# Performance work log

Hardware: AMD Instinct MI355X
Metric: run time of the kernel (lower is better)

Reference implementation:

```python
import jax, jax.numpy as jnp
import numpy as np
from jax import lax

IMG_SIZE = 640
STRIDES = (8, 16, 32)
NA = 3          # anchors per level
NC = 80         # classes
CONF_THRESH = 0.001
NMS_THRESH = 0.6
ANCHORS = np.array([[10,13],[16,30],[33,23],[30,61],[62,45],[59,119],[116,90],[156,198],[373,326]], np.float32).reshape(3, 3, 2)

def _make_grids():
    gs, st, aw = [], [], []
    for i, s in enumerate(STRIDES):
        hs = ws = IMG_SIZE // s
        gy, gx = np.meshgrid(np.arange(hs), np.arange(ws), indexing='ij')
        gxy = np.stack([gx, gy], -1).astype(np.float32).reshape(1, hs*ws, 1, 2)
        gs.append(gxy)
        st.append(np.full((1, hs*ws, NA, 2), s, np.float32))
        aw.append(np.tile(ANCHORS[i][None], (hs*ws, 1, 1)))
    return (np.concatenate(gs, 1), np.concatenate(st, 1), np.concatenate(aw, 0)[None])

GRID_CELL, STRIDE_T, ANCH_WH = _make_grids()  # [1,HW,1,2], [1,HW,3,2], [1,HW,3,2]

def _nms_classaware(boxes, score, valid):
    # Greedy NMS, class-aware via coordinate offset already applied to boxes.
    # Faithful to the numpy baseline: w,h = max(1e-28, .), areas without +1.
    x1, y1, x2, y2 = boxes[:, 0], boxes[:, 1], boxes[:, 2], boxes[:, 3]
    areas = (x2 - x1) * (y2 - y1)
    order = jnp.argsort(-score)
    N = boxes.shape[0]
    def body(i, state):
        supp, keep = state
        idx = order[i]
        active = jnp.logical_and(jnp.logical_not(supp[idx]), valid[idx])
        keep = keep.at[idx].set(active)
        xx1 = jnp.maximum(x1[idx], x1)
        yy1 = jnp.maximum(y1[idx], y1)
        xx2 = jnp.minimum(x2[idx], x2)
        yy2 = jnp.minimum(y2[idx], y2)
        w = jnp.maximum(1e-28, xx2 - xx1)
        h = jnp.maximum(1e-28, yy2 - yy1)
        inter = w * h
        iou = inter / (areas[idx] + areas - inter)
        newsupp = jnp.logical_and(iou > NMS_THRESH, active)
        newsupp = newsupp.at[idx].set(False)
        return jnp.logical_or(supp, newsupp), keep
    supp0 = jnp.zeros((N,), bool)
    keep0 = jnp.zeros((N,), bool)
    _, keep = lax.fori_loop(0, N, body, (supp0, keep0))
    return keep

def _decode_and_nms(pred_s, pred_m, pred_l):
    objs, clss, regs = [], [], []
    for pred in (pred_s, pred_m, pred_l):
        B, C, H, W = pred.shape
        p = pred.transpose(0, 2, 3, 1).reshape(B, H*W, C)
        objs.append(p[..., :NA].reshape(B, H*W*NA, 1))
        clss.append(p[..., NA:NA*(1+NC)].reshape(B, H*W*NA, NC))
        regs.append(p[..., NA*(1+NC):].reshape(B, H*W, NA, 4))
    obj_pred = jnp.concatenate(objs, axis=1)   # [B, N, 1]
    cls_pred = jnp.concatenate(clss, axis=1)   # [B, N, NC]
    reg_pred = jnp.concatenate(regs, axis=1)   # [B, HW, 3, 4]
    grid = jnp.asarray(GRID_CELL)
    stride = jnp.asarray(STRIDE_T)
    anch = jnp.asarray(ANCH_WH)
    B = reg_pred.shape[0]
    c_xy = (jax.nn.sigmoid(reg_pred[..., :2]) + grid) * stride
    b_wh = jnp.exp(reg_pred[..., 2:]) * anch
    xywh = jnp.concatenate([c_xy, b_wh], -1).reshape(B, -1, 4)
    x1y1 = xywh[..., :2] - xywh[..., 2:] / 2
    x2y2 = xywh[..., :2] + xywh[..., 2:] / 2
    boxes = jnp.clip(jnp.concatenate([x1y1, x2y2], -1) / IMG_SIZE, 0.0, 1.0)[0]  # [N,4]
    obj_s = jax.nn.sigmoid(obj_pred)[0]                     # [N,1]
    scores_all = jax.nn.softmax(cls_pred[0], axis=1) * obj_s  # [N,NC]
    cls_ind = jnp.argmax(scores_all, axis=1)                # [N]
    score = jnp.max(scores_all, axis=1)                     # [N]
    valid = score >= CONF_THRESH
    # class-aware NMS: offset normalized boxes by 2*class so classes never overlap
    boxes_off = boxes + cls_ind[:, None].astype(boxes.dtype) * 2.0
    keep = _nms_classaware(lax.stop_gradient(boxes_off), lax.stop_gradient(score), valid)
    out = jnp.concatenate([
        boxes,                                    # 4 cols
        score[:, None],                           # 1 col
        cls_ind[:, None].astype(boxes.dtype),     # 1 col (non-diff)
        keep[:, None].astype(boxes.dtype),        # 1 col (non-diff)
    ], axis=1)                                    # [N, 7]
    return out

def setup_inputs() -> dict:
    key = jax.random.key(0)
    k1, k2, k3 = jax.random.split(key, 3)
    return {
        'pred_s': jax.random.normal(k1, (1, 255, 80, 80), jnp.float32),
        'pred_m': jax.random.normal(k2, (1, 255, 40, 40), jnp.float32),
        'pred_l': jax.random.normal(k3, (1, 255, 20, 20), jnp.float32),
    }

def reference(pred_s, pred_m, pred_l):
    return _decode_and_nms(pred_s, pred_m, pred_l)
```

## Files before the change

kernel.cpp:

```cpp
#include <hip/hip_runtime.h>
#include <cstdint>

#define NPRED 25200
#define NPOS  8400
#define NCLS  80
#define CAP   512
#define MW    8
#define NCHUNK 132

__device__ __forceinline__ float sigmoidf_(float x) { return 1.0f / (1.0f + expf(-x)); }

__global__ __launch_bounds__(64, 2) void decode_kernel(
    const float* __restrict__ ps, const float* __restrict__ pm, const float* __restrict__ pl,
    float* __restrict__ out,
    float4* __restrict__ g_boxin, uint64_t* __restrict__ g_key)
{
    int chunk = blockIdx.x;
    int a     = blockIdx.y;
    int t     = threadIdx.x;

    const float* p; int HW, W, base, si; float stride; int w0;
    if (chunk < 100)      { p = ps; HW = 6400; W = 80; stride = 8.f;  base = 0;    si = 0; w0 = chunk * 64; }
    else if (chunk < 125) { p = pm; HW = 1600; W = 40; stride = 16.f; base = 6400; si = 1; w0 = (chunk - 100) * 64; }
    else                  { p = pl; HW = 400;  W = 20; stride = 32.f; base = 8000; si = 2; w0 = (chunk - 125) * 64; }

    int local = w0 + t;
    bool valid = local < HW;
    int lclamp = valid ? local : (HW - 1);

    const float* cbase = p + (size_t)(3 + a * NCLS) * HW + lclamp;
    float v[NCLS];
#pragma unroll
    for (int c = 0; c < NCLS; c++) v[c] = cbase[(size_t)c * HW];

    float objl = p[(size_t)a * HW + lclamp];
    const float* rb = p + (size_t)(3 + 3 * NCLS + a * 4) * HW + lclamp;
    float tx = rb[0], ty = rb[(size_t)HW], tw = rb[(size_t)2 * HW], th = rb[(size_t)3 * HW];

    float m = -INFINITY;
#pragma unroll
    for (int c = 0; c < NCLS; c++) m = fmaxf(m, v[c]);
    float s = 0.f; float beste = -1.f; int bi = 0;
#pragma unroll
    for (int c = 0; c < NCLS; c++) {
        float e = expf(v[c] - m);
        s += e;
        if (e > beste) { beste = e; bi = c; }
    }
    float obj = sigmoidf_(objl);
    float best = beste / s * obj;

    if (!valid) return;

    const float AW[9] = {10.f,16.f,33.f, 30.f,62.f,59.f, 116.f,156.f,373.f};
    const float AH[9] = {13.f,30.f,23.f, 61.f,45.f,119.f, 90.f,198.f,326.f};
    float aw = AW[si*3 + a], ah = AH[si*3 + a];

    int y = local / W;
    int x = local - y * W;
    float cx = (sigmoidf_(tx) + (float)x) * stride;
    float cy = (sigmoidf_(ty) + (float)y) * stride;
    float bw = expf(tw) * aw;
    float bh = expf(th) * ah;
    float x1 = fminf(fmaxf((cx - bw / 2.f) / 640.f, 0.f), 1.f);
    float y1 = fminf(fmaxf((cy - bh / 2.f) / 640.f, 0.f), 1.f);
    float x2 = fminf(fmaxf((cx + bw / 2.f) / 640.f, 0.f), 1.f);
    float y2 = fminf(fmaxf((cy + bh / 2.f) / 640.f, 0.f), 1.f);

    int g = (base + local) * 3 + a;
    float clsf = (float)bi;
    float* o = out + (size_t)g * 7;
    o[0] = x1; o[1] = y1; o[2] = x2; o[3] = y2;
    o[4] = best; o[5] = clsf; o[6] = 0.f;

    if (best >= 0.001f) {
        float off2 = clsf * 2.0f;
        g_boxin[g] = make_float4(x1 + off2, y1 + off2, x2 + off2, y2 + off2);
        unsigned u = __float_as_uint(best);
        u = (u & 0x80000000u) ? ~u : (u | 0x80000000u);
        g_key[g] = ((uint64_t)bi << 47) | ((uint64_t)(~u) << 15) | (uint64_t)g;
    } else {
        g_key[g] = (uint64_t)127 << 47;
    }
}

#define BUCKET2(kv)                                                       \
    {                                                                     \
        bool m0 = (int)((kv).x >> 47) == c;                               \
        bool m1 = (int)((kv).y >> 47) == c;                               \
        unsigned long long b0 = __ballot(m0);                             \
        unsigned long long b1 = __ballot(m1);                             \
        int total = __popcll(b0) + __popcll(b1);                          \
        int bs = 0;                                                       \
        if (lane == 0 && total) bs = atomicAdd(&ln_s, total);             \
        bs = __shfl(bs, 0);                                               \
        unsigned long long lower = ((unsigned long long)1 << lane) - 1;   \
        int off0 = bs + __popcll(b0 & lower);                             \
        int off1 = bs + __popcll(b0) + __popcll(b1 & lower);              \
        if (m0 && off0 < CAP) key_s[off0] = (kv).x;                       \
        if (m1 && off1 < CAP) key_s[off1] = (kv).y;                       \
    }

__global__ __launch_bounds__(1024, 4) void nms_fused_kernel(
    const uint64_t* __restrict__ g_key, const float4* __restrict__ g_boxin,
    float* __restrict__ out)
{
    int c = blockIdx.x;
    int tid = threadIdx.x;

    __shared__ alignas(16) uint64_t key_s[CAP];
    __shared__ float4   boxu_s[CAP];
    __shared__ float4   sbox_s[CAP + 64];
    __shared__ int      sg_s[CAP];
    __shared__ uint64_t mask_s[MW * CAP];
    __shared__ int      ln_s;

    if (tid == 0) ln_s = 0;
    __syncthreads();

    {
        int lane = tid & 63;
        const ulonglong2* kp = (const ulonglong2*)g_key;
        const int HALF = NPRED / 2;
        const int R2 = HALF >> 11;
        for (int r = 0; r < R2; r++) {
            int i0 = (r << 11) + tid;
            ulonglong2 ka = kp[i0];
            ulonglong2 kb = kp[i0 + 1024];
            BUCKET2(ka);
            BUCKET2(kb);
        }
        int ti = (R2 << 11) + tid;
        if (ti < HALF) {
            ulonglong2 ka = kp[ti];
            BUCKET2(ka);
        }
    }
    __syncthreads();
    int n = ln_s; if (n > CAP) n = CAP;
    if (n == 0) return;
    int nw = (n + 63) >> 6;

    for (int i = tid; i < n; i += 1024)
        boxu_s[i] = g_boxin[key_s[i] & 0x7FFF];
    for (int i = n + tid; i < n + 64; i += 1024)
        sbox_s[i] = make_float4(3e30f, 3e30f, 3e30f, 3e30f);
    __syncthreads();

    for (int i0 = 0; i0 < n; i0 += 256) {
        int item = i0 + (tid >> 2);
        int sub  = tid & 3;
        bool act = item < n;
        int r = 0;
        uint64_t k = 0;
        if (act) {
            k = key_s[item];
            int nq = (((n + 3) >> 2) + 1) & ~1;
            int lo = sub * nq; if (lo > n) lo = n;
            int hi = lo + nq;  if (hi > n) hi = n;
            int jj = lo;
            for (; jj + 8 <= hi; jj += 8) {
                ulonglong2 p0 = *(const ulonglong2*)&key_s[jj];
                ulonglong2 p1 = *(const ulonglong2*)&key_s[jj + 2];
                ulonglong2 p2 = *(const ulonglong2*)&key_s[jj + 4];
                ulonglong2 p3 = *(const ulonglong2*)&key_s[jj + 6];
                r += (p0.x < k) + (p0.y < k) + (p1.x < k) + (p1.y < k)
                   + (p2.x < k) + (p2.y < k) + (p3.x < k) + (p3.y < k);
            }
            for (; jj + 2 <= hi; jj += 2) {
                ulonglong2 p0 = *(const ulonglong2*)&key_s[jj];
                r += (p0.x < k) + (p0.y < k);
            }
            if (jj < hi) r += (key_s[jj] < k);
        }
        r += __shfl_xor(r, 1);
        r += __shfl_xor(r, 2);
        if (act && sub == 0) {
            sbox_s[r] = boxu_s[item];
            sg_s[r]   = (int)(k & 0x7FFF);
        }
    }
    __syncthreads();

    {
        int wid   = tid >> 6;
        int lane2 = tid & 63;
        int T = nw * (nw + 1) / 2;
        for (int t = wid; t < T; t += 16) {
            int w = 0, acc = 0;
            while (t >= acc + w + 1) { acc += w + 1; w++; }
            int ib = t - acc;
            int i  = (ib << 6) + lane2;
            float4 b4 = sbox_s[i];
            float Ai = (b4.z - b4.x) * (b4.w - b4.y);
            int j0 = w << 6;
            float4 bjc = sbox_s[j0];
            uint64_t bits = 0;
#pragma unroll 8
            for (int jq = 0; jq < 64; jq++) {
                float4 bjn = sbox_s[j0 + ((jq + 1) & 63)];
                float xx1 = fmaxf(b4.x, bjc.x);
                float yy1 = fmaxf(b4.y, bjc.y);
                float xx2 = fminf(b4.z, bjc.z);
                float yy2 = fminf(b4.w, bjc.w);
                float ww = fmaxf(1e-28f, xx2 - xx1);
                float hh = fmaxf(1e-28f, yy2 - yy1);
                float inter = ww * hh;
                float Aj = (bjc.z - bjc.x) * (bjc.w - bjc.y);
                float iou = inter / ((Ai + Aj) - inter);
                if ((j0 + jq) > i && iou > 0.6f) bits |= 1ull << jq;
                bjc = bjn;
            }
            if (i < n) mask_s[w * CAP + i] = bits;
        }
    }
    __syncthreads();

    if (tid >= 64) return;
    int lane = tid;
    uint64_t removed = 0;
    for (int w = 0; w < nw; w++) {
        uint64_t rw = __shfl(removed, w);
        int row = (w << 6) + lane;
        uint64_t diag = (row < n) ? mask_s[w * CAP + row] : 0ull;
        int rem = n - (w << 6);
        uint64_t valid = (rem >= 64) ? ~0ull : ((1ull << rem) - 1ull);
        uint64_t nulls = __ballot(diag == 0ull);
        uint64_t cand = ~rw & valid;
        uint64_t kw = 0;
        uint64_t it = cand & ~nulls;
        while (it) {
            int b = __ffsll((unsigned long long)it) - 1;
            kw |= 1ull << b;
            uint64_t db = __shfl(diag, b);
            it &= ~db; cand &= ~db;
            it &= ~(1ull << b);
        }
        kw |= cand & nulls;

        int g  = lane >> 3;
        int wp = lane & 7;
        uint64_t acc = 0;
        if (wp >= w && wp < nw) {
            int rbase = (w << 6) + (g << 3);
#pragma unroll
            for (int bb = 0; bb < 8; bb++) {
                uint64_t mword = mask_s[wp * CAP + rbase + bb];
                if ((kw >> ((g << 3) + bb)) & 1) acc |= mword;
            }
        }
        acc |= __shfl_xor(acc, 8);
        acc |= __shfl_xor(acc, 16);
        acc |= __shfl_xor(acc, 32);
        if (lane < MW) removed |= acc;

        if (row < n && ((kw >> lane) & 1))
            out[(size_t)sg_s[row] * 7 + 6] = 1.0f;
    }
}

extern "C" void kernel_launch(void* const* d_in, const int* in_sizes, int n_in,
                              void* d_out, int out_size, void* d_ws, size_t ws_size,
                              hipStream_t stream) {
    const float* ps = (const float*)d_in[0];
    const float* pm = (const float*)d_in[1];
    const float* pl = (const float*)d_in[2];
    float* out = (float*)d_out;

    char* ws = (char*)d_ws;
    float4*   g_boxin = (float4*)ws;
    uint64_t* g_key   = (uint64_t*)(ws + 409600);

    decode_kernel<<<dim3(NCHUNK, 3), 64, 0, stream>>>(ps, pm, pl, out, g_boxin, g_key);
    nms_fused_kernel<<<NCLS, 1024, 0, stream>>>(g_key, g_boxin, out);
}
```

Measured before the change: 101.6 us.

## Replace atomic ballot bucketing with two-pass count and prefix-scan compaction; batch IoU loads

Per-class key gathering no longer uses per-wavefront ballots and shared atomics. Each thread counts its matches, a wave and block prefix scan assigns offsets, and a second pass over global keys writes them deterministically. The IoU mask loop also loads eight boxes from LDS at once before computing, which adds ILP. The cost is reading the key array from global memory twice and more register pressure from the full unroll.

```diff
diff --git a/kernel.cpp b/kernel.cpp
--- a/kernel.cpp
+++ b/kernel.cpp
@@ -84,21 +84,18 @@
     }
 }
 
-#define BUCKET2(kv)                                                       \
-    {                                                                     \
-        bool m0 = (int)((kv).x >> 47) == c;                               \
-        bool m1 = (int)((kv).y >> 47) == c;                               \
-        unsigned long long b0 = __ballot(m0);                             \
-        unsigned long long b1 = __ballot(m1);                             \
-        int total = __popcll(b0) + __popcll(b1);                          \
-        int bs = 0;                                                       \
-        if (lane == 0 && total) bs = atomicAdd(&ln_s, total);             \
-        bs = __shfl(bs, 0);                                               \
-        unsigned long long lower = ((unsigned long long)1 << lane) - 1;   \
-        int off0 = bs + __popcll(b0 & lower);                             \
-        int off1 = bs + __popcll(b0) + __popcll(b1 & lower);              \
-        if (m0 && off0 < CAP) key_s[off0] = (kv).x;                       \
-        if (m1 && off1 < CAP) key_s[off1] = (kv).y;                       \
+#define IOUBIT(BJ, JQ)                                                   \
+    {                                                                    \
+        float xx1 = fmaxf(b4.x, (BJ).x);                                 \
+        float yy1 = fmaxf(b4.y, (BJ).y);                                 \
+        float xx2 = fminf(b4.z, (BJ).z);                                 \
+        float yy2 = fminf(b4.w, (BJ).w);                                 \
+        float ww = fmaxf(1e-28f, xx2 - xx1);                             \
+        float hh = fmaxf(1e-28f, yy2 - yy1);                             \
+        float inter = ww * hh;                                           \
+        float Aj = ((BJ).z - (BJ).x) * ((BJ).w - (BJ).y);                \
+        float iou = inter / ((Ai + Aj) - inter);                         \
+        if ((j0 + (JQ)) > i && iou > 0.6f) bits |= 1ull << (JQ);         \
     }
 
 __global__ __launch_bounds__(1024, 4) void nms_fused_kernel(
@@ -107,37 +104,58 @@
 {
     int c = blockIdx.x;
     int tid = threadIdx.x;
+    int wid  = tid >> 6;
+    int lane = tid & 63;
 
     __shared__ alignas(16) uint64_t key_s[CAP];
     __shared__ float4   boxu_s[CAP];
     __shared__ float4   sbox_s[CAP + 64];
     __shared__ int      sg_s[CAP];
     __shared__ uint64_t mask_s[MW * CAP];
-    __shared__ int      ln_s;
-
-    if (tid == 0) ln_s = 0;
-    __syncthreads();
+    __shared__ int      wsum[16];
+
+    const ulonglong2* kp = (const ulonglong2*)g_key;
+    const int HALF = NPRED / 2;
+    int cnt = 0;
+#pragma unroll
+    for (int j = 0; j < 13; j++) {
+        int idx = j * 1024 + tid;
+        if (idx < HALF) {
+            ulonglong2 kv = kp[idx];
+            cnt += ((int)(kv.x >> 47) == c) + ((int)(kv.y >> 47) == c);
+        }
+    }
+    int pre = cnt;
+#pragma unroll
+    for (int d = 1; d < 64; d <<= 1) {
+        int vv = __shfl_up(pre, d);
+        if (lane >= d) pre += vv;
+    }
+    if (lane == 63) wsum[wid] = pre;
+    __syncthreads();
+    int wbase = 0, ntot = 0;
+#pragma unroll
+    for (int wq = 0; wq < 16; wq++) {
+        int t16 = wsum[wq];
+        if (wq < wid) wbase += t16;
+        ntot += t16;
+    }
+    int base = wbase + pre - cnt;
 
     {
-        int lane = tid & 63;
-        const ulonglong2* kp = (const ulonglong2*)g_key;
-        const int HALF = NPRED / 2;
-        const int R2 = HALF >> 11;
-        for (int r = 0; r < R2; r++) {
-            int i0 = (r << 11) + tid;
-            ulonglong2 ka = kp[i0];
-            ulonglong2 kb = kp[i0 + 1024];
-            BUCKET2(ka);
-            BUCKET2(kb);
-        }
-        int ti = (R2 << 11) + tid;
-        if (ti < HALF) {
-            ulonglong2 ka = kp[ti];
-            BUCKET2(ka);
-        }
-    }
-    __syncthreads();
-    int n = ln_s; if (n > CAP) n = CAP;
+        int wr = base;
+#pragma unroll
+        for (int j = 0; j < 13; j++) {
+            int idx = j * 1024 + tid;
+            if (idx < HALF) {
+                ulonglong2 kv = kp[idx];
+                if ((int)(kv.x >> 47) == c && wr < CAP) key_s[wr++] = kv.x;
+                if ((int)(kv.y >> 47) == c && wr < CAP) key_s[wr++] = kv.y;
+            }
+        }
+    }
+    __syncthreads();
+    int n = ntot; if (n > CAP) n = CAP;
     if (n == 0) return;
     int nw = (n + 63) >> 6;
 
@@ -183,33 +201,30 @@
     __syncthreads();
 
     {
-        int wid   = tid >> 6;
-        int lane2 = tid & 63;
         int T = nw * (nw + 1) / 2;
         for (int t = wid; t < T; t += 16) {
             int w = 0, acc = 0;
             while (t >= acc + w + 1) { acc += w + 1; w++; }
             int ib = t - acc;
-            int i  = (ib << 6) + lane2;
+            int i  = (ib << 6) + lane;
             float4 b4 = sbox_s[i];
             float Ai = (b4.z - b4.x) * (b4.w - b4.y);
             int j0 = w << 6;
-            float4 bjc = sbox_s[j0];
             uint64_t bits = 0;
-#pragma unroll 8
-            for (int jq = 0; jq < 64; jq++) {
-                float4 bjn = sbox_s[j0 + ((jq + 1) & 63)];
-                float xx1 = fmaxf(b4.x, bjc.x);
-                float yy1 = fmaxf(b4.y, bjc.y);
-                float xx2 = fminf(b4.z, bjc.z);
-                float yy2 = fminf(b4.w, bjc.w);
-                float ww = fmaxf(1e-28f, xx2 - xx1);
-                float hh = fmaxf(1e-28f, yy2 - yy1);
-                float inter = ww * hh;
-                float Aj = (bjc.z - bjc.x) * (bjc.w - bjc.y);
-                float iou = inter / ((Ai + Aj) - inter);
-                if ((j0 + jq) > i && iou > 0.6f) bits |= 1ull << jq;
-                bjc = bjn;
+#pragma unroll
+            for (int jq0 = 0; jq0 < 64; jq0 += 8) {
+                float4 q0 = sbox_s[j0 + jq0 + 0];
+                float4 q1 = sbox_s[j0 + jq0 + 1];
+                float4 q2 = sbox_s[j0 + jq0 + 2];
+                float4 q3 = sbox_s[j0 + jq0 + 3];
+                float4 q4 = sbox_s[j0 + jq0 + 4];
+                float4 q5 = sbox_s[j0 + jq0 + 5];
+                float4 q6 = sbox_s[j0 + jq0 + 6];
+                float4 q7 = sbox_s[j0 + jq0 + 7];
+                IOUBIT(q0, jq0 + 0); IOUBIT(q1, jq0 + 1);
+                IOUBIT(q2, jq0 + 2); IOUBIT(q3, jq0 + 3);
+                IOUBIT(q4, jq0 + 4); IOUBIT(q5, jq0 + 5);
+                IOUBIT(q6, jq0 + 6); IOUBIT(q7, jq0 + 7);
             }
             if (i < n) mask_s[w * CAP + i] = bits;
         }
@@ -217,7 +232,6 @@
     __syncthreads();
 
     if (tid >= 64) return;
-    int lane = tid;
     uint64_t removed = 0;
     for (int w = 0; w < nw; w++) {
         uint64_t rw = __shfl(removed, w);
```

Result: no change. 101.4 us (-0.2%).
